# Performance work log

Hardware: AMD Instinct MI355X
Metric: run time of the kernel (lower is better)

The kernel has to match this reference:

```python
import jax, jax.numpy as jnp
import numpy as np

BATCH = 131072
STATE_DIM = 64
CONTROL_DIM = 16
HIDDEN = 256
ALPHA = 0.1
MAX_ITERS = 200
TOL = 0.01
TRACKED_ITERS = 5
U_MIN, U_MAX = -1.0, 1.0


def setup_inputs() -> dict:
    key = jax.random.key(0)
    ks = jax.random.split(key, 8)
    def w(k, shape, fan_in):
        return (jax.random.normal(k, shape, jnp.float32) / np.float32(np.sqrt(fan_in)))
    x = jax.random.normal(ks[0], (BATCH, STATE_DIM), jnp.float32)
    t = jax.random.uniform(ks[1], (1,), jnp.float32)
    W1 = w(ks[2], (STATE_DIM + 1, HIDDEN), STATE_DIM + 1)
    b1 = jnp.zeros((HIDDEN,), jnp.float32)
    W2 = w(ks[3], (HIDDEN, HIDDEN), HIDDEN)
    b2 = jnp.zeros((HIDDEN,), jnp.float32)
    W3 = w(ks[4], (HIDDEN, STATE_DIM), HIDDEN)
    b3 = jnp.zeros((STATE_DIM,), jnp.float32)
    Bmat = w(ks[5], (STATE_DIM, CONTROL_DIM), STATE_DIM)  # oc_problem dynamics matrix
    return {"x": x, "t": t, "W1": W1, "b1": b1, "W2": W2, "b2": b2,
            "W3": W3, "b3": b3, "Bmat": Bmat}


def _p_net(t, x, W1, b1, W2, b2, W3, b3):
    # DefaultPNet: pad x with scalar t, then 3-layer ReLU MLP -> p in [B, state_dim]
    n = x.shape[0]
    tcol = jnp.broadcast_to(t.reshape(1, 1).astype(x.dtype), (n, 1))
    zt = jnp.concatenate([x, tcol], axis=1)
    h = jax.nn.relu(zt @ W1 + b1)
    h = jax.nn.relu(h @ W2 + b2)
    return h @ W3 + b3


def reference(x, t, W1, b1, W2, b2, W3, b3, Bmat):
    # grad_H_u(t,x,u,p) = u + p @ Bmat  (LQ Hamiltonian); p independent of u,
    # so p is computed once (same math as recomputing it every iteration).
    p = _p_net(t, x, W1, b1, W2, b2, W3, b3)          # [B, state_dim]
    pB = p @ Bmat                                      # [B, control_dim]
    clamp = lambda u: jnp.clip(u, U_MIN, U_MAX)
    T = lambda u, pb: u - ALPHA * (u + pb)

    u0 = jnp.zeros((x.shape[0], CONTROL_DIM), x.dtype)
    pB_ng = jax.lax.stop_gradient(pB)

    def cond(st):
        _, i, res = st
        return (res >= TOL) & (i < MAX_ITERS)

    def body(st):
        u, i, _ = st
        u_new = clamp(T(u, pB_ng))
        res = jnp.max(jnp.linalg.norm(u_new - u, axis=1)) / ALPHA
        return (u_new, i + 1, res)

    u_fp, _, _ = jax.lax.while_loop(cond, body, (u0, jnp.int32(0), jnp.float32(jnp.inf)))

    # training path: tracked_iters differentiable refinement steps + final T
    u = jax.lax.stop_gradient(u_fp)
    for _ in range(TRACKED_ITERS + 1):
        u = clamp(T(u, pB))
    return u
```

## Files before the change

### kernel.cpp

```cpp
#include <hip/hip_runtime.h>


typedef __bf16 bf16;
typedef __bf16 bf16x8 __attribute__((ext_vector_type(8)));
typedef __bf16 bf16x4 __attribute__((ext_vector_type(4)));
typedef float  f32x4  __attribute__((ext_vector_type(4)));

#define HID    256
#define SDIM   64
#define CDIM   16
#define BM     128
#define GRID   256
#define ITERS  4
#define LDH    264
#define LDX    72

#define MFMA(a, b, c) __builtin_amdgcn_mfma_f32_16x16x32_bf16(a, b, c, 0, 0, 0)

__device__ __forceinline__ int sh_idx(int row, int h) { return row * LDH + h; }

__global__ __launch_bounds__(512, 2)
void oc_main(const float* __restrict__ x,  const float* __restrict__ t,
             const float* __restrict__ W1, const float* __restrict__ b1,
             const float* __restrict__ W2, const float* __restrict__ b2,
             const float* __restrict__ W3, const float* __restrict__ b3,
             const float* __restrict__ Bmat, float* __restrict__ out) {
  __shared__ bf16 sH1[BM * LDH];
  __shared__ bf16 sH2[BM * LDH];
  __shared__ bf16 sX [BM * LDX];
  const int tid  = threadIdx.x;
  const int wave = tid >> 6, lane = tid & 63;
  const int q    = lane >> 4, l = lane & 15;

  auto stage = [&](int tile) {
    const float* xp = x + (size_t)tile * BM * SDIM;
#pragma unroll
    for (int i = 0; i < 4; ++i) {
      const int e = i * 512 + tid;
      const int r = e >> 4, k4 = (e & 15) * 4;
      const float4 v = *(const float4*)(xp + r * SDIM + k4);
      bf16x4 w = {(bf16)v.x, (bf16)v.y, (bf16)v.z, (bf16)v.w};
      *(bf16x4*)(&sX[r * LDX + k4]) = w;
    }
  };

  {
    const int n1 = tid >> 1;
    const int cb = (tid & 1) * 8;
    float aw[8];
#pragma unroll
    for (int i = 0; i < 8; ++i) aw[i] = 0.f;
    for (int m = 0; m < SDIM; ++m) {
      const float w = W3[n1 * SDIM + m];
      const float4 bA = *(const float4*)(&Bmat[m * CDIM + cb]);
      const float4 bB = *(const float4*)(&Bmat[m * CDIM + cb + 4]);
      aw[0] = fmaf(w, bA.x, aw[0]); aw[1] = fmaf(w, bA.y, aw[1]);
      aw[2] = fmaf(w, bA.z, aw[2]); aw[3] = fmaf(w, bA.w, aw[3]);
      aw[4] = fmaf(w, bB.x, aw[4]); aw[5] = fmaf(w, bB.y, aw[5]);
      aw[6] = fmaf(w, bB.z, aw[6]); aw[7] = fmaf(w, bB.w, aw[7]);
    }
    const int kt = n1 >> 5, qq = (n1 >> 3) & 3, jj = n1 & 7;
#pragma unroll
    for (int ci = 0; ci < 8; ++ci)
      sH1[(kt * 64 + qq * 16 + cb + ci) * 8 + jj] = (bf16)aw[ci];
  }
  stage(blockIdx.x);
  __syncthreads();

  bf16x8 W3t[8];
#pragma unroll
  for (int kt = 0; kt < 8; ++kt)
    W3t[kt] = *(const bf16x8*)(&sH1[(kt * 64 + lane) * 8]);

  bf16x8 W1t[2][2], W2t[8][2];
#pragma unroll
  for (int kt = 0; kt < 2; ++kt)
#pragma unroll
    for (int mt = 0; mt < 2; ++mt) {
      bf16x8 v;
#pragma unroll
      for (int j = 0; j < 8; ++j)
        v[j] = (bf16)W1[(32 * kt + 8 * q + j) * HID + 32 * wave + 16 * mt + l];
      W1t[kt][mt] = v;
    }
#pragma unroll
  for (int kt = 0; kt < 8; ++kt)
#pragma unroll
    for (int mt = 0; mt < 2; ++mt) {
      bf16x8 v;
#pragma unroll
      for (int j = 0; j < 8; ++j)
        v[j] = (bf16)W2[(32 * kt + 8 * q + j) * HID + 32 * wave + 16 * mt + l];
      W2t[kt][mt] = v;
    }

  const float tt = t[0];
  f32x4 b1e[2], b2e[2];
#pragma unroll
  for (int mt = 0; mt < 2; ++mt)
#pragma unroll
    for (int r = 0; r < 4; ++r) {
      const int h = 32 * wave + 16 * mt + 4 * q + r;
      b1e[mt][r] = b1[h] + tt * W1[SDIM * HID + h];
      b2e[mt][r] = b2[h];
    }
  f32x4 b3t = (f32x4){0.f, 0.f, 0.f, 0.f};
  for (int m = 0; m < SDIM; ++m) {
    const float bm = b3[m];
    const float4 v = *(const float4*)(&Bmat[m * CDIM + 4 * q]);
    b3t[0] = fmaf(bm, v.x, b3t[0]); b3t[1] = fmaf(bm, v.y, b3t[1]);
    b3t[2] = fmaf(bm, v.z, b3t[2]); b3t[3] = fmaf(bm, v.w, b3t[3]);
  }
  __syncthreads();

  f32x4 acc[2][8];

  for (int it = 0; it < ITERS; ++it) {
    const int tile = blockIdx.x + it * GRID;

#pragma unroll
    for (int mt = 0; mt < 2; ++mt)
#pragma unroll
      for (int nt = 0; nt < 8; ++nt) acc[mt][nt] = (f32x4){0.f, 0.f, 0.f, 0.f};
#pragma unroll
    for (int kt = 0; kt < 2; ++kt)
#pragma unroll
      for (int nt = 0; nt < 8; ++nt) {
        const bf16x8 b = *(const bf16x8*)(&sX[(16 * nt + l) * LDX + 32 * kt + 8 * q]);
        acc[0][nt] = MFMA(W1t[kt][0], b, acc[0][nt]);
        acc[1][nt] = MFMA(W1t[kt][1], b, acc[1][nt]);
      }
#pragma unroll
    for (int mt = 0; mt < 2; ++mt) {
      const int h0 = 32 * wave + 16 * mt + 4 * q;
#pragma unroll
      for (int nt = 0; nt < 8; ++nt) {
        bf16x4 v;
#pragma unroll
        for (int r = 0; r < 4; ++r) v[r] = (bf16)fmaxf(acc[mt][nt][r] + b1e[mt][r], 0.f);
        *(bf16x4*)(&sH1[sh_idx(16 * nt + l, h0)]) = v;
      }
    }
    __syncthreads();

#pragma unroll
    for (int mt = 0; mt < 2; ++mt)
#pragma unroll
      for (int nt = 0; nt < 8; ++nt) acc[mt][nt] = (f32x4){0.f, 0.f, 0.f, 0.f};
#pragma unroll
    for (int kt = 0; kt < 8; ++kt)
#pragma unroll
      for (int nt = 0; nt < 8; ++nt) {
        const bf16x8 b = *(const bf16x8*)(&sH1[sh_idx(16 * nt + l, 32 * kt + 8 * q)]);
        acc[0][nt] = MFMA(W2t[kt][0], b, acc[0][nt]);
        acc[1][nt] = MFMA(W2t[kt][1], b, acc[1][nt]);
      }
    if (it + 1 < ITERS) stage(tile + GRID);
    __syncthreads();

#pragma unroll
    for (int mt = 0; mt < 2; ++mt) {
      const int h0 = 32 * wave + 16 * mt + 4 * q;
#pragma unroll
      for (int nt = 0; nt < 8; ++nt) {
        bf16x4 hi, lo;
#pragma unroll
        for (int r = 0; r < 4; ++r) {
          const float v = fmaxf(acc[mt][nt][r] + b2e[mt][r], 0.f);
          const bf16 h = (bf16)v;
          hi[r] = h;
          lo[r] = (bf16)(v - (float)h);
        }
        const int idx = sh_idx(16 * nt + l, h0);
        *(bf16x4*)(&sH2[idx]) = hi;
        *(bf16x4*)(&sH1[idx]) = lo;
      }
    }
    __syncthreads();

    f32x4 a3 = (f32x4){0.f, 0.f, 0.f, 0.f};
#pragma unroll
    for (int kt = 0; kt < 8; ++kt) {
      const int idx = sh_idx(16 * wave + l, 32 * kt + 8 * q);
      const bf16x8 bh = *(const bf16x8*)(&sH2[idx]);
      const bf16x8 bl = *(const bf16x8*)(&sH1[idx]);
      a3 = MFMA(W3t[kt], bh, a3);
      a3 = MFMA(W3t[kt], bl, a3);
    }
    f32x4 o;
#pragma unroll
    for (int r = 0; r < 4; ++r)
      o[r] = fminf(fmaxf(-(a3[r] + b3t[r]), -1.f), 1.f);
    *(float4*)(&out[((size_t)tile * BM + 16 * wave + l) * CDIM + 4 * q]) = *(float4*)&o;

    __syncthreads();
  }
}

extern "C" void kernel_launch(void* const* d_in, const int* in_sizes, int n_in,
                              void* d_out, int out_size, void* d_ws, size_t ws_size,
                              hipStream_t stream) {
  const float* x    = (const float*)d_in[0];
  const float* t    = (const float*)d_in[1];
  const float* W1   = (const float*)d_in[2];
  const float* b1   = (const float*)d_in[3];
  const float* W2   = (const float*)d_in[4];
  const float* b2   = (const float*)d_in[5];
  const float* W3   = (const float*)d_in[6];
  const float* b3   = (const float*)d_in[7];
  const float* Bmat = (const float*)d_in[8];
  float* out = (float*)d_out;
  (void)d_ws; (void)ws_size;

  hipLaunchKernelGGL(oc_main, dim3(GRID), dim3(512), 0, stream,
                     x, t, W1, b1, W2, b2, W3, b3, Bmat, out);
}
```

Measured before the change: 129.1 us.

## Halve tile rows, split final layer and next-tile staging across waves

Tile size drops from 128 to 64 rows and the grid doubles, with launch bounds raised to ask for four blocks per CU. The fused W3·B matrix is now written by every block to a global workspace and read back in layer 3, instead of being held in registers. Layer 3 runs on waves 0-3 while waves 4-7 load the next x tile, so staging overlaps the final MFMA. Biases are folded into the accumulator initialisation. The tighter launch bound may force register spilling, since W2 fragments alone need many VGPRs, and LDS use likely still blocks four resident blocks.

After: 227.5 us. 76.2% more time.

```diff
diff --git a/kernel.cpp b/kernel.cpp
--- a/kernel.cpp
+++ b/kernel.cpp
@@ -9,8 +9,8 @@
 #define HID    256
 #define SDIM   64
 #define CDIM   16
-#define BM     128
-#define GRID   256
+#define BM     64
+#define GRID   512
 #define ITERS  4
 #define LDH    264
 #define LDX    72
@@ -19,12 +19,13 @@
 
 __device__ __forceinline__ int sh_idx(int row, int h) { return row * LDH + h; }
 
-__global__ __launch_bounds__(512, 2)
+__global__ __launch_bounds__(512, 4)
 void oc_main(const float* __restrict__ x,  const float* __restrict__ t,
              const float* __restrict__ W1, const float* __restrict__ b1,
              const float* __restrict__ W2, const float* __restrict__ b2,
              const float* __restrict__ W3, const float* __restrict__ b3,
-             const float* __restrict__ Bmat, float* __restrict__ out) {
+             const float* __restrict__ Bmat, bf16* __restrict__ w3ws,
+             float* __restrict__ out) {
   __shared__ bf16 sH1[BM * LDH];
   __shared__ bf16 sH2[BM * LDH];
   __shared__ bf16 sX [BM * LDX];
@@ -32,45 +33,35 @@
   const int wave = tid >> 6, lane = tid & 63;
   const int q    = lane >> 4, l = lane & 15;
 
-  auto stage = [&](int tile) {
-    const float* xp = x + (size_t)tile * BM * SDIM;
-#pragma unroll
-    for (int i = 0; i < 4; ++i) {
+  {
+    const int kt = tid >> 6, fl = tid & 63;
+    const int r0 = kt * 32 + ((fl >> 4) << 3);
+    const int c  = fl & 15;
+    float aw[8];
+#pragma unroll
+    for (int j = 0; j < 8; ++j) aw[j] = 0.f;
+    for (int m = 0; m < SDIM; ++m) {
+      const float bm = Bmat[m * CDIM + c];
+#pragma unroll
+      for (int j = 0; j < 8; ++j) aw[j] = fmaf(W3[(r0 + j) * SDIM + m], bm, aw[j]);
+    }
+    bf16x8 v;
+#pragma unroll
+    for (int j = 0; j < 8; ++j) v[j] = (bf16)aw[j];
+    *(bf16x8*)(w3ws + (size_t)tid * 8) = v;
+  }
+
+  {
+    const float* xp = x + (size_t)blockIdx.x * BM * SDIM;
+#pragma unroll
+    for (int i = 0; i < 2; ++i) {
       const int e = i * 512 + tid;
       const int r = e >> 4, k4 = (e & 15) * 4;
       const float4 v = *(const float4*)(xp + r * SDIM + k4);
       bf16x4 w = {(bf16)v.x, (bf16)v.y, (bf16)v.z, (bf16)v.w};
       *(bf16x4*)(&sX[r * LDX + k4]) = w;
     }
-  };
-
-  {
-    const int n1 = tid >> 1;
-    const int cb = (tid & 1) * 8;
-    float aw[8];
-#pragma unroll
-    for (int i = 0; i < 8; ++i) aw[i] = 0.f;
-    for (int m = 0; m < SDIM; ++m) {
-      const float w = W3[n1 * SDIM + m];
-      const float4 bA = *(const float4*)(&Bmat[m * CDIM + cb]);
-      const float4 bB = *(const float4*)(&Bmat[m * CDIM + cb + 4]);
-      aw[0] = fmaf(w, bA.x, aw[0]); aw[1] = fmaf(w, bA.y, aw[1]);
-      aw[2] = fmaf(w, bA.z, aw[2]); aw[3] = fmaf(w, bA.w, aw[3]);
-      aw[4] = fmaf(w, bB.x, aw[4]); aw[5] = fmaf(w, bB.y, aw[5]);
-      aw[6] = fmaf(w, bB.z, aw[6]); aw[7] = fmaf(w, bB.w, aw[7]);
-    }
-    const int kt = n1 >> 5, qq = (n1 >> 3) & 3, jj = n1 & 7;
-#pragma unroll
-    for (int ci = 0; ci < 8; ++ci)
-      sH1[(kt * 64 + qq * 16 + cb + ci) * 8 + jj] = (bf16)aw[ci];
-  }
-  stage(blockIdx.x);
-  __syncthreads();
-
-  bf16x8 W3t[8];
-#pragma unroll
-  for (int kt = 0; kt < 8; ++kt)
-    W3t[kt] = *(const bf16x8*)(&sH1[(kt * 64 + lane) * 8]);
+  }
 
   bf16x8 W1t[2][2], W2t[8][2];
 #pragma unroll
@@ -104,7 +95,9 @@
       b1e[mt][r] = b1[h] + tt * W1[SDIM * HID + h];
       b2e[mt][r] = b2[h];
     }
-  f32x4 b3t = (f32x4){0.f, 0.f, 0.f, 0.f};
+  f32x4 b3t;
+#pragma unroll
+  for (int r = 0; r < 4; ++r) b3t[r] = 0.f;
   for (int m = 0; m < SDIM; ++m) {
     const float bm = b3[m];
     const float4 v = *(const float4*)(&Bmat[m * CDIM + 4 * q]);
@@ -113,7 +106,7 @@
   }
   __syncthreads();
 
-  f32x4 acc[2][8];
+  f32x4 acc[2][4];
 
   for (int it = 0; it < ITERS; ++it) {
     const int tile = blockIdx.x + it * GRID;
@@ -121,11 +114,11 @@
 #pragma unroll
     for (int mt = 0; mt < 2; ++mt)
 #pragma unroll
-      for (int nt = 0; nt < 8; ++nt) acc[mt][nt] = (f32x4){0.f, 0.f, 0.f, 0.f};
+      for (int nt = 0; nt < 4; ++nt) acc[mt][nt] = b1e[mt];
 #pragma unroll
     for (int kt = 0; kt < 2; ++kt)
 #pragma unroll
-      for (int nt = 0; nt < 8; ++nt) {
+      for (int nt = 0; nt < 4; ++nt) {
         const bf16x8 b = *(const bf16x8*)(&sX[(16 * nt + l) * LDX + 32 * kt + 8 * q]);
         acc[0][nt] = MFMA(W1t[kt][0], b, acc[0][nt]);
         acc[1][nt] = MFMA(W1t[kt][1], b, acc[1][nt]);
@@ -134,10 +127,10 @@
     for (int mt = 0; mt < 2; ++mt) {
       const int h0 = 32 * wave + 16 * mt + 4 * q;
 #pragma unroll
-      for (int nt = 0; nt < 8; ++nt) {
+      for (int nt = 0; nt < 4; ++nt) {
         bf16x4 v;
 #pragma unroll
-        for (int r = 0; r < 4; ++r) v[r] = (bf16)fmaxf(acc[mt][nt][r] + b1e[mt][r], 0.f);
+        for (int r = 0; r < 4; ++r) v[r] = (bf16)fmaxf(acc[mt][nt][r], 0.f);
         *(bf16x4*)(&sH1[sh_idx(16 * nt + l, h0)]) = v;
       }
     }
@@ -146,27 +139,26 @@
 #pragma unroll
     for (int mt = 0; mt < 2; ++mt)
 #pragma unroll
-      for (int nt = 0; nt < 8; ++nt) acc[mt][nt] = (f32x4){0.f, 0.f, 0.f, 0.f};
+      for (int nt = 0; nt < 4; ++nt) acc[mt][nt] = b2e[mt];
 #pragma unroll
     for (int kt = 0; kt < 8; ++kt)
 #pragma unroll
-      for (int nt = 0; nt < 8; ++nt) {
+      for (int nt = 0; nt < 4; ++nt) {
         const bf16x8 b = *(const bf16x8*)(&sH1[sh_idx(16 * nt + l, 32 * kt + 8 * q)]);
         acc[0][nt] = MFMA(W2t[kt][0], b, acc[0][nt]);
         acc[1][nt] = MFMA(W2t[kt][1], b, acc[1][nt]);
       }
-    if (it + 1 < ITERS) stage(tile + GRID);
     __syncthreads();
 
 #pragma unroll
     for (int mt = 0; mt < 2; ++mt) {
       const int h0 = 32 * wave + 16 * mt + 4 * q;
 #pragma unroll
-      for (int nt = 0; nt < 8; ++nt) {
+      for (int nt = 0; nt < 4; ++nt) {
         bf16x4 hi, lo;
 #pragma unroll
         for (int r = 0; r < 4; ++r) {
-          const float v = fmaxf(acc[mt][nt][r] + b2e[mt][r], 0.f);
+          const float v = fmaxf(acc[mt][nt][r], 0.f);
           const bf16 h = (bf16)v;
           hi[r] = h;
           lo[r] = (bf16)(v - (float)h);
@@ -178,21 +170,34 @@
     }
     __syncthreads();
 
-    f32x4 a3 = (f32x4){0.f, 0.f, 0.f, 0.f};
-#pragma unroll
-    for (int kt = 0; kt < 8; ++kt) {
-      const int idx = sh_idx(16 * wave + l, 32 * kt + 8 * q);
-      const bf16x8 bh = *(const bf16x8*)(&sH2[idx]);
-      const bf16x8 bl = *(const bf16x8*)(&sH1[idx]);
-      a3 = MFMA(W3t[kt], bh, a3);
-      a3 = MFMA(W3t[kt], bl, a3);
-    }
-    f32x4 o;
-#pragma unroll
-    for (int r = 0; r < 4; ++r)
-      o[r] = fminf(fmaxf(-(a3[r] + b3t[r]), -1.f), 1.f);
-    *(float4*)(&out[((size_t)tile * BM + 16 * wave + l) * CDIM + 4 * q]) = *(float4*)&o;
-
+    if (wave < 4) {
+      f32x4 a3 = b3t;
+#pragma unroll
+      for (int kt = 0; kt < 8; ++kt) {
+        const bf16x8 w3 = *(const bf16x8*)(w3ws + ((size_t)kt * 64 + lane) * 8);
+        const int idx = sh_idx(16 * wave + l, 32 * kt + 8 * q);
+        const bf16x8 bh = *(const bf16x8*)(&sH2[idx]);
+        const bf16x8 bl = *(const bf16x8*)(&sH1[idx]);
+        a3 = MFMA(w3, bh, a3);
+        a3 = MFMA(w3, bl, a3);
+      }
+      f32x4 o;
+#pragma unroll
+      for (int r = 0; r < 4; ++r)
+        o[r] = fminf(fmaxf(-a3[r], -1.f), 1.f);
+      *(float4*)(&out[((size_t)tile * BM + 16 * wave + l) * CDIM + 4 * q]) = *(float4*)&o;
+    } else if (it + 1 < ITERS) {
+      const float* xp = x + (size_t)(tile + GRID) * BM * SDIM;
+      const int tid2 = tid - 256;
+#pragma unroll
+      for (int i = 0; i < 4; ++i) {
+        const int e = i * 256 + tid2;
+        const int r = e >> 4, k4 = (e & 15) * 4;
+        const float4 v = *(const float4*)(xp + r * SDIM + k4);
+        bf16x4 w = {(bf16)v.x, (bf16)v.y, (bf16)v.z, (bf16)v.w};
+        *(bf16x4*)(&sX[r * LDX + k4]) = w;
+      }
+    }
     __syncthreads();
   }
 }
@@ -210,8 +215,8 @@
   const float* b3   = (const float*)d_in[7];
   const float* Bmat = (const float*)d_in[8];
   float* out = (float*)d_out;
-  (void)d_ws; (void)ws_size;
+  bf16*  w3ws = (bf16*)d_ws;
 
   hipLaunchKernelGGL(oc_main, dim3(GRID), dim3(512), 0, stream,
-                     x, t, W1, b1, W2, b2, W3, b3, Bmat, out);
+                     x, t, W1, b1, W2, b2, W3, b3, Bmat, w3ws, out);
 }
```
